# Kernel optimization log

Hardware: AMD Instinct MI355X
Metric: run time of the kernel (lower is better)

Reference implementation:

```python
import jax, jax.numpy as jnp
import numpy as np

N = 50000
E = 800000
D_IN, D_HID, D_OUT = 128, 128, 64


def setup_inputs() -> dict:
    key = jax.random.key(0)
    ks = jax.random.split(key, 8)
    x = jax.random.normal(ks[0], (N, D_IN), dtype=jnp.float32)
    edge_index = jax.random.randint(ks[1], (2, E), 0, N, dtype=jnp.int64)
    # SAGEConv params: lin_l (neighbors, with bias), lin_r (root, no bias)
    s1 = 1.0 / np.sqrt(D_IN)
    s2 = 1.0 / np.sqrt(D_HID)
    W1_l = jax.random.uniform(ks[2], (D_IN, D_HID), jnp.float32, -s1, s1)
    b1 = jnp.zeros((D_HID,), jnp.float32)
    W1_r = jax.random.uniform(ks[3], (D_IN, D_HID), jnp.float32, -s1, s1)
    W2_l = jax.random.uniform(ks[4], (D_HID, D_OUT), jnp.float32, -s2, s2)
    b2 = jnp.zeros((D_OUT,), jnp.float32)
    W2_r = jax.random.uniform(ks[5], (D_HID, D_OUT), jnp.float32, -s2, s2)
    return {"x": x, "edge_index": edge_index, "W1_l": W1_l, "b1": b1,
            "W1_r": W1_r, "W2_l": W2_l, "b2": b2, "W2_r": W2_r}


def _sage_conv(x, src, dst, Wl, b, Wr, num_nodes):
    # mean aggregation over incoming edges (src -> dst)
    msgs = x[src]                                              # [E, d]
    agg = jax.ops.segment_sum(msgs, dst, num_segments=num_nodes)
    cnt = jax.ops.segment_sum(jnp.ones((src.shape[0],), x.dtype), dst,
                              num_segments=num_nodes)
    mean = agg / jnp.clip(cnt, 1.0)[:, None]                   # [N, d]
    return mean @ Wl + b + x @ Wr


def reference(x, edge_index, W1_l, b1, W1_r, W2_l, b2, W2_r):
    src, dst = edge_index[0], edge_index[1]
    n = x.shape[0]
    h = jax.nn.relu(_sage_conv(x, src, dst, W1_l, b1, W1_r, n))
    # dropout p=0.5 is identity in eval mode (training=False)
    return _sage_conv(h, src, dst, W2_l, b2, W2_r, n)
```

## Files before the change

kernel.cpp:

```cpp
#include <hip/hip_runtime.h>
#include <hip/hip_bf16.h>

typedef __hip_bfloat16 bf16;
typedef __attribute__((ext_vector_type(8))) short short8;
typedef __attribute__((ext_vector_type(4))) float floatx4;
typedef __attribute__((ext_vector_type(2))) float floatx2;
typedef unsigned short u16;
typedef unsigned char u8;

#define NNODES 50000
#define NEDGES 800000
#define D_IN  128
#define D_HID 128
#define D_OUT 64
#define NBLK  ((NNODES + 255) / 256)

__device__ __forceinline__ float bfbits2f(unsigned int u) {
    return __uint_as_float(u << 16);
}
__device__ __forceinline__ float b2f(bf16 v) { return __bfloat162float(v); }
__device__ __forceinline__ unsigned short f2bfbits(float f) {
    bf16 b = __float2bfloat16(f);
    return *(unsigned short*)&b;
}
__device__ __forceinline__ u8 f2fp8(float f) {
    return (u8)(__builtin_amdgcn_cvt_pk_fp8_f32(f, 0.f, 0, false) & 0xFF);
}
__device__ __forceinline__ float ld(const void* p, long long idx, int isf32) {
    if (isf32) return ((const float*)p)[idx];
    return b2f(((const bf16*)p)[idx]);
}

__global__ void k_setup(int* __restrict__ cnt, int n,
                        const unsigned int* __restrict__ ei_words,
                        const unsigned int* __restrict__ w_words,
                        int* __restrict__ flags,
                        const void* __restrict__ x,
                        const void* __restrict__ W1l, const void* __restrict__ W1r,
                        const void* __restrict__ W2l, const void* __restrict__ W2r,
                        bf16* __restrict__ p1l, bf16* __restrict__ p1r,
                        bf16* __restrict__ p2l, bf16* __restrict__ p2r,
                        unsigned int* __restrict__ x8) {
    int b = blockIdx.x;
    if (b < 128) {
        if (b == 0) {
            __shared__ int cnt_zero, cnt_bf;
            if (threadIdx.x == 0) { cnt_zero = 0; cnt_bf = 0; }
            __syncthreads();
            int t = threadIdx.x;
            unsigned int we = ei_words[2 * t + 1];
            if (we == 0u) atomicAdd(&cnt_zero, 1);
            unsigned int ww = w_words[t];
            unsigned int lowexp = (ww >> 7) & 0xFFu;
            if (lowexp >= 0x60u && lowexp <= 0x7Bu) atomicAdd(&cnt_bf, 1);
            __syncthreads();
            if (threadIdx.x == 0) {
                flags[0] = (cnt_zero >= 240) ? 1 : 0;
                flags[1] = (cnt_bf >= 192) ? 0 : 1;
            }
        }
        int i = b * blockDim.x + threadIdx.x;
        int stride = 128 * blockDim.x;
        for (; i < n; i += stride) cnt[i] = 0;
        return;
    }
    __shared__ int cnt_bf2;
    if (threadIdx.x == 0) cnt_bf2 = 0;
    __syncthreads();
    {
        unsigned int ww = w_words[threadIdx.x];
        unsigned int lowexp = (ww >> 7) & 0xFFu;
        if (lowexp >= 0x60u && lowexp <= 0x7Bu) atomicAdd(&cnt_bf2, 1);
    }
    __syncthreads();
    int isf32 = (cnt_bf2 >= 192) ? 0 : 1;
    if (b < 152) {
        int t = (b - 128) * 256 + threadIdx.x;
        if (t >= 6144) return;
        const void* Wm; bf16* dst; int NT; int base;
        if (t < 2048)      { Wm = W1l; dst = p1l; NT = 8; base = t; }
        else if (t < 4096) { Wm = W1r; dst = p1r; NT = 8; base = t - 2048; }
        else if (t < 5120) { Wm = W2l; dst = p2l; NT = 4; base = t - 4096; }
        else               { Wm = W2r; dst = p2r; NT = 4; base = t - 5120; }
        int lane = base & 63;
        int kt = (base >> 6) & 3;
        int nt = base >> 8;
        int Nmat = NT * 16;
        int krow = kt * 32 + ((lane >> 4) * 8);
        int col = nt * 16 + (lane & 15);
        #pragma unroll
        for (int j = 0; j < 8; j++) {
            float v = ld(Wm, (long long)(krow + j) * Nmat + col, isf32);
            dst[(((nt * 4 + kt) * 64 + lane) * 8) + j] = __float2bfloat16(v);
        }
        return;
    }
    const long long NU32 = (long long)NNODES * D_IN / 4;
    long long i = (long long)(b - 152) * 256 + threadIdx.x;
    long long stride = (long long)(gridDim.x - 152) * 256;
    if (isf32) {
        const float4* xf = (const float4*)x;
        for (; i < NU32; i += stride) {
            float4 f = xf[i];
            unsigned int w0 = __builtin_amdgcn_cvt_pk_fp8_f32(f.x, f.y, 0, false);
            w0 = __builtin_amdgcn_cvt_pk_fp8_f32(f.z, f.w, w0, true);
            x8[i] = w0;
        }
    } else {
        const ushort4* xb = (const ushort4*)x;
        for (; i < NU32; i += stride) {
            ushort4 s = xb[i];
            float f0 = bfbits2f(s.x), f1 = bfbits2f(s.y);
            float f2 = bfbits2f(s.z), f3 = bfbits2f(s.w);
            unsigned int w0 = __builtin_amdgcn_cvt_pk_fp8_f32(f0, f1, 0, false);
            w0 = __builtin_amdgcn_cvt_pk_fp8_f32(f2, f3, w0, true);
            x8[i] = w0;
        }
    }
}

__global__ void k_edges(const int* __restrict__ ei, const int* __restrict__ flags,
                        u16* __restrict__ src16, unsigned int* __restrict__ drpack,
                        int* __restrict__ cnt) {
    int e = blockIdx.x * blockDim.x + threadIdx.x;
    if (e >= NEDGES) return;
    int s, d;
    if (flags[0]) { s = ei[2 * e]; d = ei[2 * (NEDGES + e)]; }
    else          { s = ei[e];     d = ei[NEDGES + e]; }
    src16[e] = (u16)s;
    int rank = atomicAdd(&cnt[d], 1);
    drpack[e] = ((unsigned int)rank << 16) | (unsigned int)d;
}

__global__ void k_scan_a(const int* __restrict__ cnt, int* __restrict__ excl,
                         int* __restrict__ bsum) {
    __shared__ int s[256];
    int t = threadIdx.x;
    int i = blockIdx.x * 256 + t;
    int v = (i < NNODES) ? cnt[i] : 0;
    s[t] = v;
    __syncthreads();
    for (int off = 1; off < 256; off <<= 1) {
        int u = (t >= off) ? s[t - off] : 0;
        __syncthreads();
        s[t] += u;
        __syncthreads();
    }
    if (i < NNODES) excl[i] = s[t] - v;
    if (t == 255) bsum[blockIdx.x] = s[255];
}

__global__ void k_scan_bc(const int* __restrict__ excl, const int* __restrict__ bsum,
                          int* __restrict__ row_start) {
    __shared__ int s[256];
    __shared__ int bo;
    int t = threadIdx.x;
    int v = (t < NBLK) ? bsum[t] : 0;
    s[t] = v;
    __syncthreads();
    for (int off = 1; off < 256; off <<= 1) {
        int u = (t >= off) ? s[t - off] : 0;
        __syncthreads();
        s[t] += u;
        __syncthreads();
    }
    if (t == 0) bo = s[blockIdx.x] - bsum[blockIdx.x];
    __syncthreads();
    int i = blockIdx.x * 256 + t;
    if (i < NNODES) row_start[i] = bo + excl[i];
    if (i == 0) row_start[NNODES] = NEDGES;
}

__global__ void k_scatter(const u16* __restrict__ src16,
                          const unsigned int* __restrict__ drpack,
                          const int* __restrict__ row_start,
                          u16* __restrict__ csr16) {
    int e = blockIdx.x * blockDim.x + threadIdx.x;
    if (e >= NEDGES) return;
    unsigned int dp = drpack[e];
    int d = (int)(dp & 0xFFFFu);
    int r = (int)(dp >> 16);
    csr16[row_start[d] + r] = src16[e];
}

__device__ __forceinline__ void g16m(const unsigned int* __restrict__ x8w, int my,
                                     int j, int cnt2, int h, int c,
                                     float& a0, float& a1, float& a2, float& a3) {
    int jb = j + h * 8;
    int i0 = __shfl(my, jb + 0), i1 = __shfl(my, jb + 1);
    int i2 = __shfl(my, jb + 2), i3 = __shfl(my, jb + 3);
    int i4 = __shfl(my, jb + 4), i5 = __shfl(my, jb + 5);
    int i6 = __shfl(my, jb + 6), i7 = __shfl(my, jb + 7);
    unsigned int u0 = x8w[((unsigned)i0 << 5) + c];
    unsigned int u1 = x8w[((unsigned)i1 << 5) + c];
    unsigned int u2 = x8w[((unsigned)i2 << 5) + c];
    unsigned int u3 = x8w[((unsigned)i3 << 5) + c];
    unsigned int u4 = x8w[((unsigned)i4 << 5) + c];
    unsigned int u5 = x8w[((unsigned)i5 << 5) + c];
    unsigned int u6 = x8w[((unsigned)i6 << 5) + c];
    unsigned int u7 = x8w[((unsigned)i7 << 5) + c];
    float m0 = (jb + 0 < cnt2) ? 1.f : 0.f;
    float m1 = (jb + 1 < cnt2) ? 1.f : 0.f;
    float m2 = (jb + 2 < cnt2) ? 1.f : 0.f;
    float m3 = (jb + 3 < cnt2) ? 1.f : 0.f;
    float m4 = (jb + 4 < cnt2) ? 1.f : 0.f;
    float m5 = (jb + 5 < cnt2) ? 1.f : 0.f;
    float m6 = (jb + 6 < cnt2) ? 1.f : 0.f;
    float m7 = (jb + 7 < cnt2) ? 1.f : 0.f;
    floatx2 l0 = __builtin_amdgcn_cvt_pk_f32_fp8(u0, false);
    floatx2 h0 = __builtin_amdgcn_cvt_pk_f32_fp8(u0, true);
    floatx2 l1 = __builtin_amdgcn_cvt_pk_f32_fp8(u1, false);
    floatx2 h1 = __builtin_amdgcn_cvt_pk_f32_fp8(u1, true);
    floatx2 l2 = __builtin_amdgcn_cvt_pk_f32_fp8(u2, false);
    floatx2 h2 = __builtin_amdgcn_cvt_pk_f32_fp8(u2, true);
    floatx2 l3 = __builtin_amdgcn_cvt_pk_f32_fp8(u3, false);
    floatx2 h3 = __builtin_amdgcn_cvt_pk_f32_fp8(u3, true);
    floatx2 l4 = __builtin_amdgcn_cvt_pk_f32_fp8(u4, false);
    floatx2 h4 = __builtin_amdgcn_cvt_pk_f32_fp8(u4, true);
    floatx2 l5 = __builtin_amdgcn_cvt_pk_f32_fp8(u5, false);
    floatx2 h5 = __builtin_amdgcn_cvt_pk_f32_fp8(u5, true);
    floatx2 l6 = __builtin_amdgcn_cvt_pk_f32_fp8(u6, false);
    floatx2 h6 = __builtin_amdgcn_cvt_pk_f32_fp8(u6, true);
    floatx2 l7 = __builtin_amdgcn_cvt_pk_f32_fp8(u7, false);
    floatx2 h7 = __builtin_amdgcn_cvt_pk_f32_fp8(u7, true);
    a0 += m0 * l0.x; a1 += m0 * l0.y; a2 += m0 * h0.x; a3 += m0 * h0.y;
    a0 += m1 * l1.x; a1 += m1 * l1.y; a2 += m1 * h1.x; a3 += m1 * h1.y;
    a0 += m2 * l2.x; a1 += m2 * l2.y; a2 += m2 * h2.x; a3 += m2 * h2.y;
    a0 += m3 * l3.x; a1 += m3 * l3.y; a2 += m3 * h3.x; a3 += m3 * h3.y;
    a0 += m4 * l4.x; a1 += m4 * l4.y; a2 += m4 * h4.x; a3 += m4 * h4.y;
    a0 += m5 * l5.x; a1 += m5 * l5.y; a2 += m5 * h5.x; a3 += m5 * h5.y;
    a0 += m6 * l6.x; a1 += m6 * l6.y; a2 += m6 * h6.x; a3 += m6 * h6.y;
    a0 += m7 * l7.x; a1 += m7 * l7.y; a2 += m7 * h7.x; a3 += m7 * h7.y;
}

__global__ __launch_bounds__(512) void k_l1fused(
        const int* __restrict__ row_start, const u16* __restrict__ csr16,
        const void* __restrict__ x, const unsigned int* __restrict__ x8w,
        const int* __restrict__ flags,
        const bf16* __restrict__ p1l, const bf16* __restrict__ p1r,
        const bf16* __restrict__ p2l, const bf16* __restrict__ p2r,
        const void* __restrict__ b1, const void* __restrict__ b2v,
        u8* __restrict__ h28, float* __restrict__ hrf) {
    __shared__ bf16 ms[16][136];
    __shared__ bf16 xs[16][136];
    __shared__ bf16 hs[16][136];
    __shared__ u8 h2s8[16][72];
    __shared__ float hrs[16][68];
    int t = threadIdx.x;
    int w = t >> 6;
    int l = t & 63;
    int nb = blockIdx.x * 16;
    int isf32 = flags[1];
    int r0 = w * 2, r1 = r0 + 1;
    int h = l >> 5;
    int c = l & 31;

    int rsv = row_start[nb + r0 + min(l, 2)];
    int s0 = __shfl(rsv, 0), s1 = __shfl(rsv, 1), s2 = __shfl(rsv, 2);

    int ca = min(64, s1 - s0);
    int cb = min(64, s2 - s1);
    int mya = (l < ca) ? (int)csr16[s0 + l] : 0;
    int myb = (l < cb) ? (int)csr16[s1 + l] : 0;

    {
        long long ro0 = (long long)(nb + r0) * D_IN + 2 * l;
        long long ro1 = (long long)(nb + r1) * D_IN + 2 * l;
        unsigned int px0, px1;
        if (isf32) {
            float2 v0 = *(const float2*)((const float*)x + ro0);
            float2 v1 = *(const float2*)((const float*)x + ro1);
            px0 = ((unsigned int)f2bfbits(v0.y) << 16) | f2bfbits(v0.x);
            px1 = ((unsigned int)f2bfbits(v1.y) << 16) | f2bfbits(v1.x);
        } else {
            px0 = *(const unsigned int*)((const bf16*)x + ro0);
            px1 = *(const unsigned int*)((const bf16*)x + ro1);
        }
        *(unsigned int*)((bf16*)&xs[r0][0] + 2 * l) = px0;
        *(unsigned int*)((bf16*)&xs[r1][0] + 2 * l) = px1;
    }

    float aa0 = 0.f, aa1 = 0.f, aa2 = 0.f, aa3 = 0.f;
    float bb0 = 0.f, bb1 = 0.f, bb2 = 0.f, bb3 = 0.f;
    {
        int mx = max(ca, cb);
        for (int j = 0; j < mx; j += 16) {
            g16m(x8w, mya, j, ca, h, c, aa0, aa1, aa2, aa3);
            g16m(x8w, myb, j, cb, h, c, bb0, bb1, bb2, bb3);
        }
    }
    for (int base = s0 + 64; base < s1; base += 64) {
        int cnt2 = min(64, s1 - base);
        int my = (l < cnt2) ? (int)csr16[base + l] : 0;
        for (int j = 0; j < cnt2; j += 16) g16m(x8w, my, j, cnt2, h, c, aa0, aa1, aa2, aa3);
    }
    for (int base = s1 + 64; base < s2; base += 64) {
        int cnt2 = min(64, s2 - base);
        int my = (l < cnt2) ? (int)csr16[base + l] : 0;
        for (int j = 0; j < cnt2; j += 16) g16m(x8w, my, j, cnt2, h, c, bb0, bb1, bb2, bb3);
    }
    aa0 += __shfl_xor(aa0, 32); aa1 += __shfl_xor(aa1, 32);
    aa2 += __shfl_xor(aa2, 32); aa3 += __shfl_xor(aa3, 32);
    bb0 += __shfl_xor(bb0, 32); bb1 += __shfl_xor(bb1, 32);
    bb2 += __shfl_xor(bb2, 32); bb3 += __shfl_xor(bb3, 32);
    if (l < 32) {
        float inv = 1.0f / fmaxf((float)(s1 - s0), 1.0f);
        uint2 pk;
        pk.x = ((unsigned int)f2bfbits(aa1 * inv) << 16) | f2bfbits(aa0 * inv);
        pk.y = ((unsigned int)f2bfbits(aa3 * inv) << 16) | f2bfbits(aa2 * inv);
        *(uint2*)((bf16*)&ms[r0][0] + (c << 2)) = pk;
    } else {
        float inv = 1.0f / fmaxf((float)(s2 - s1), 1.0f);
        uint2 pk;
        pk.x = ((unsigned int)f2bfbits(bb1 * inv) << 16) | f2bfbits(bb0 * inv);
        pk.y = ((unsigned int)f2bfbits(bb3 * inv) << 16) | f2bfbits(bb2 * inv);
        *(uint2*)((bf16*)&ms[r1][0] + (c << 2)) = pk;
    }
    __syncthreads();

    int m = l & 15;
    int quad = l >> 4;
    floatx4 acc0 = {0.f, 0.f, 0.f, 0.f};
    #pragma unroll
    for (int kt = 0; kt < 4; kt++) {
        short8 amv = *(const short8*)&ms[m][kt * 32 + quad * 8];
        short8 axv = *(const short8*)&xs[m][kt * 32 + quad * 8];
        short8 bl0 = *(const short8*)(p1l + (((w * 4 + kt) * 64 + l) * 8));
        short8 br0 = *(const short8*)(p1r + (((w * 4 + kt) * 64 + l) * 8));
        acc0 = __builtin_amdgcn_mfma_f32_16x16x32_bf16(amv, bl0, acc0, 0, 0, 0);
        acc0 = __builtin_amdgcn_mfma_f32_16x16x32_bf16(axv, br0, acc0, 0, 0, 0);
    }
    int c0 = w * 16 + m;
    float bias0 = ld(b1, c0, isf32);
    #pragma unroll
    for (int r = 0; r < 4; r++) {
        hs[quad * 4 + r][c0] = __float2bfloat16(fmaxf(acc0[r] + bias0, 0.f));
    }
    __syncthreads();
    if (w < 4) {
        floatx4 acc2 = {0.f, 0.f, 0.f, 0.f};
        floatx4 acc3 = {0.f, 0.f, 0.f, 0.f};
        #pragma unroll
        for (int kt = 0; kt < 4; kt++) {
            short8 ah = *(const short8*)&hs[m][kt * 32 + quad * 8];
            short8 bw = *(const short8*)(p2l + (((w * 4 + kt) * 64 + l) * 8));
            short8 bz = *(const short8*)(p2r + (((w * 4 + kt) * 64 + l) * 8));
            acc2 = __builtin_amdgcn_mfma_f32_16x16x32_bf16(ah, bw, acc2, 0, 0, 0);
            acc3 = __builtin_amdgcn_mfma_f32_16x16x32_bf16(ah, bz, acc3, 0, 0, 0);
        }
        int c2 = w * 16 + m;
        float bias2 = ld(b2v, c2, isf32);
        #pragma unroll
        for (int r = 0; r < 4; r++) {
            h2s8[quad * 4 + r][c2] = f2fp8(acc2[r]);
            hrs[quad * 4 + r][c2] = acc3[r] + bias2;
        }
    }
    __syncthreads();
    if (t < 128) {
        int node = t >> 3, col0 = (t & 7) * 8;
        uint2 v = *(const uint2*)&h2s8[node][col0];
        *(uint2*)(h28 + (long long)(nb + node) * D_OUT + col0) = v;
    }
    if (t < 256) {
        int node = t >> 4, col0 = (t & 15) * 4;
        float4 v = *(const float4*)&hrs[node][col0];
        *(float4*)(hrf + (long long)(nb + node) * D_OUT + col0) = v;
    }
}

__device__ __forceinline__ void a16m(const unsigned int* __restrict__ h32, int my,
                                     int j, int cnt2, int g, int c,
                                     float& a0, float& a1, float& a2, float& a3) {
    int jj0 = j + g, jj1 = j + 4 + g, jj2 = j + 8 + g, jj3 = j + 12 + g;
    int i0 = __shfl(my, jj0);
    int i1 = __shfl(my, jj1);
    int i2 = __shfl(my, jj2);
    int i3 = __shfl(my, jj3);
    unsigned int u0 = h32[(size_t)i0 * 16 + c];
    unsigned int u1 = h32[(size_t)i1 * 16 + c];
    unsigned int u2 = h32[(size_t)i2 * 16 + c];
    unsigned int u3 = h32[(size_t)i3 * 16 + c];
    float m0 = (jj0 < cnt2) ? 1.f : 0.f;
    float m1 = (jj1 < cnt2) ? 1.f : 0.f;
    float m2 = (jj2 < cnt2) ? 1.f : 0.f;
    float m3 = (jj3 < cnt2) ? 1.f : 0.f;
    floatx2 l0 = __builtin_amdgcn_cvt_pk_f32_fp8(u0, false);
    floatx2 h0 = __builtin_amdgcn_cvt_pk_f32_fp8(u0, true);
    floatx2 l1 = __builtin_amdgcn_cvt_pk_f32_fp8(u1, false);
    floatx2 h1 = __builtin_amdgcn_cvt_pk_f32_fp8(u1, true);
    floatx2 l2 = __builtin_amdgcn_cvt_pk_f32_fp8(u2, false);
    floatx2 h2 = __builtin_amdgcn_cvt_pk_f32_fp8(u2, true);
    floatx2 l3 = __builtin_amdgcn_cvt_pk_f32_fp8(u3, false);
    floatx2 h3 = __builtin_amdgcn_cvt_pk_f32_fp8(u3, true);
    a0 += m0 * l0.x; a1 += m0 * l0.y; a2 += m0 * h0.x; a3 += m0 * h0.y;
    a0 += m1 * l1.x; a1 += m1 * l1.y; a2 += m1 * h1.x; a3 += m1 * h1.y;
    a0 += m2 * l2.x; a1 += m2 * l2.y; a2 += m2 * h2.x; a3 += m2 * h2.y;
    a0 += m3 * l3.x; a1 += m3 * l3.y; a2 += m3 * h3.x; a3 += m3 * h3.y;
}

__global__ void k_agg2g(const int* __restrict__ row_start, const u16* __restrict__ csr16,
                        const u8* __restrict__ h28, const float* __restrict__ hrf,
                        const int* __restrict__ flags, void* __restrict__ out) {
    int t = threadIdx.x;
    int lane = t & 63;
    int n0 = blockIdx.x * 8 + (t >> 6) * 2;
    int n1 = n0 + 1;
    int g = lane >> 4;
    int c = lane & 15;
    const unsigned int* h32 = (const unsigned int*)h28;

    int rsv = row_start[n0 + min(lane, 2)];
    int s0 = __shfl(rsv, 0), s1 = __shfl(rsv, 1), s2 = __shfl(rsv, 2);
    int ca = min(64, s1 - s0);
    int cb = min(64, s2 - s1);
    int mya = (lane < ca) ? (int)csr16[s0 + lane] : 0;
    int myb = (lane < cb) ? (int)csr16[s1 + lane] : 0;

    float4 hr = {0.f, 0.f, 0.f, 0.f};
    if (lane < 32) {
        int nn = (lane < 16) ? n0 : n1;
        hr = *(const float4*)&hrf[(size_t)nn * D_OUT + (c << 2)];
    }

    float a0 = 0.f, a1 = 0.f, a2 = 0.f, a3 = 0.f;
    float b0 = 0.f, b1 = 0.f, b2 = 0.f, b3 = 0.f;
    {
        int mx = max(ca, cb);
        for (int j = 0; j < mx; j += 16) {
            a16m(h32, mya, j, ca, g, c, a0, a1, a2, a3);
            a16m(h32, myb, j, cb, g, c, b0, b1, b2, b3);
        }
    }
    for (int base = s0 + 64; base < s1; base += 64) {
        int cnt2 = min(64, s1 - base);
        int my = (lane < cnt2) ? (int)csr16[base + lane] : 0;
        for (int j = 0; j < cnt2; j += 16) a16m(h32, my, j, cnt2, g, c, a0, a1, a2, a3);
    }
    for (int base = s1 + 64; base < s2; base += 64) {
        int cnt2 = min(64, s2 - base);
        int my = (lane < cnt2) ? (int)csr16[base + lane] : 0;
        for (int j = 0; j < cnt2; j += 16) a16m(h32, my, j, cnt2, g, c, b0, b1, b2, b3);
    }
    a0 += __shfl_xor(a0, 32); a0 += __shfl_xor(a0, 16);
    a1 += __shfl_xor(a1, 32); a1 += __shfl_xor(a1, 16);
    a2 += __shfl_xor(a2, 32); a2 += __shfl_xor(a2, 16);
    a3 += __shfl_xor(a3, 32); a3 += __shfl_xor(a3, 16);
    b0 += __shfl_xor(b0, 32); b0 += __shfl_xor(b0, 16);
    b1 += __shfl_xor(b1, 32); b1 += __shfl_xor(b1, 16);
    b2 += __shfl_xor(b2, 32); b2 += __shfl_xor(b2, 16);
    b3 += __shfl_xor(b3, 32); b3 += __shfl_xor(b3, 16);
    if (lane < 16) {
        float inv = 1.0f / fmaxf((float)(s1 - s0), 1.0f);
        float o0 = a0 * inv + hr.x;
        float o1 = a1 * inv + hr.y;
        float o2 = a2 * inv + hr.z;
        float o3 = a3 * inv + hr.w;
        if (flags[1]) {
            float4 v = {o0, o1, o2, o3};
            *(float4*)((float*)out + (size_t)n0 * D_OUT + (c << 2)) = v;
        } else {
            uint2 v;
            v.x = ((unsigned int)f2bfbits(o1) << 16) | f2bfbits(o0);
            v.y = ((unsigned int)f2bfbits(o3) << 16) | f2bfbits(o2);
            *(uint2*)((bf16*)out + (size_t)n0 * D_OUT + (c << 2)) = v;
        }
    } else if (lane < 32) {
        float inv = 1.0f / fmaxf((float)(s2 - s1), 1.0f);
        float o0 = b0 * inv + hr.x;
        float o1 = b1 * inv + hr.y;
        float o2 = b2 * inv + hr.z;
        float o3 = b3 * inv + hr.w;
        if (flags[1]) {
            float4 v = {o0, o1, o2, o3};
            *(float4*)((float*)out + (size_t)n1 * D_OUT + (c << 2)) = v;
        } else {
            uint2 v;
            v.x = ((unsigned int)f2bfbits(o1) << 16) | f2bfbits(o0);
            v.y = ((unsigned int)f2bfbits(o3) << 16) | f2bfbits(o2);
            *(uint2*)((bf16*)out + (size_t)n1 * D_OUT + (c << 2)) = v;
        }
    }
}

extern "C" void kernel_launch(void* const* d_in, const int* in_sizes, int n_in,
                              void* d_out, int out_size, void* d_ws, size_t ws_size,
                              hipStream_t stream) {
    const void* x   = d_in[0];
    const int*  ei  = (const int*)d_in[1];
    const void* W1l = d_in[2];
    const void* b1  = d_in[3];
    const void* W1r = d_in[4];
    const void* W2l = d_in[5];
    const void* b2v = d_in[6];
    const void* W2r = d_in[7];

    const int N = NNODES;
    const int E = NEDGES;

    int*          flags     = (int*)d_ws;
    u16*          src16     = (u16*)(flags + 4);
    unsigned int* drpack    = (unsigned int*)(src16 + E);
    int*          cnt       = (int*)(drpack + E);
    int*          excl      = cnt + N;
    int*          bsum      = excl + N;
    int*          row_start = bsum + 256;
    u16*          csr16     = (u16*)(row_start + (N + 16));
    bf16*         p1l       = (bf16*)(csr16 + E);
    bf16*         p1r       = p1l + 16384;
    bf16*         p2l       = p1r + 16384;
    bf16*         p2r       = p2l + 8192;
    unsigned int* x8        = (unsigned int*)(p2r + 8192);
    u8*           h28       = (u8*)(x8 + (size_t)N * D_IN / 4);
    float*        hrf       = (float*)(h28 + (size_t)N * D_OUT);

    k_setup<<<152 + 1024, 256, 0, stream>>>(cnt, N, (const unsigned int*)ei,
                                            (const unsigned int*)W1l, flags, x,
                                            W1l, W1r, W2l, W2r,
                                            p1l, p1r, p2l, p2r, x8);
    k_edges<<<(E + 255) / 256, 256, 0, stream>>>(ei, flags, src16, drpack, cnt);
    k_scan_a<<<NBLK, 256, 0, stream>>>(cnt, excl, bsum);
    k_scan_bc<<<NBLK, 256, 0, stream>>>(excl, bsum, row_start);
    k_scatter<<<(E + 255) / 256, 256, 0, stream>>>(src16, drpack, row_start, csr16);
    k_l1fused<<<N / 16, 512, 0, stream>>>(row_start, csr16, x, x8, flags,
                                          p1l, p1r, p2l, p2r, b1, b2v, h28, hrf);
    k_agg2g<<<N / 8, 256, 0, stream>>>(row_start, csr16, h28, hrf, flags, d_out);
}
```

Measured before the change: 196.2 us.

## Process two node tiles per layer-1 block and four nodes per warp in aggregation

The fused layer-1 kernel now handles two 16-node tiles per block, prefetching the second tile's row starts, neighbor indices and root features while the first tile's MFMA work runs, which halves the block count and reuses weight loads. The layer-2 aggregation kernel gives each warp four destination nodes instead of two, issuing more independent gathers per loop iteration for memory-level parallelism. The cost is higher register pressure and longer serial work per block, which may reduce occupancy and worsen load imbalance on high-degree nodes.

```diff
diff --git a/kernel.cpp b/kernel.cpp
--- a/kernel.cpp
+++ b/kernel.cpp
@@ -249,23 +249,25 @@
     int t = threadIdx.x;
     int w = t >> 6;
     int l = t & 63;
-    int nb = blockIdx.x * 16;
     int isf32 = flags[1];
     int r0 = w * 2, r1 = r0 + 1;
     int h = l >> 5;
     int c = l & 31;
-
-    int rsv = row_start[nb + r0 + min(l, 2)];
+    int m = l & 15;
+    int quad = l >> 4;
+    int nbA = blockIdx.x * 32;
+    int nbB = nbA + 16;
+    bool hasB = (nbB < NNODES);
+
+    int rsv = row_start[nbA + r0 + min(l, 2)];
     int s0 = __shfl(rsv, 0), s1 = __shfl(rsv, 1), s2 = __shfl(rsv, 2);
-
     int ca = min(64, s1 - s0);
     int cb = min(64, s2 - s1);
     int mya = (l < ca) ? (int)csr16[s0 + l] : 0;
     int myb = (l < cb) ? (int)csr16[s1 + l] : 0;
-
     {
-        long long ro0 = (long long)(nb + r0) * D_IN + 2 * l;
-        long long ro1 = (long long)(nb + r1) * D_IN + 2 * l;
+        long long ro0 = (long long)(nbA + r0) * D_IN + 2 * l;
+        long long ro1 = (long long)(nbA + r1) * D_IN + 2 * l;
         unsigned int px0, px1;
         if (isf32) {
             float2 v0 = *(const float2*)((const float*)x + ro0);
@@ -299,6 +301,10 @@
         int my = (l < cnt2) ? (int)csr16[base + l] : 0;
         for (int j = 0; j < cnt2; j += 16) g16m(x8w, my, j, cnt2, h, c, bb0, bb1, bb2, bb3);
     }
+
+    int rsvB = 0;
+    if (hasB) rsvB = row_start[nbB + r0 + min(l, 2)];
+
     aa0 += __shfl_xor(aa0, 32); aa1 += __shfl_xor(aa1, 32);
     aa2 += __shfl_xor(aa2, 32); aa3 += __shfl_xor(aa3, 32);
     bb0 += __shfl_xor(bb0, 32); bb1 += __shfl_xor(bb1, 32);
@@ -318,23 +324,45 @@
     }
     __syncthreads();
 
-    int m = l & 15;
-    int quad = l >> 4;
-    floatx4 acc0 = {0.f, 0.f, 0.f, 0.f};
-    #pragma unroll
-    for (int kt = 0; kt < 4; kt++) {
-        short8 amv = *(const short8*)&ms[m][kt * 32 + quad * 8];
-        short8 axv = *(const short8*)&xs[m][kt * 32 + quad * 8];
-        short8 bl0 = *(const short8*)(p1l + (((w * 4 + kt) * 64 + l) * 8));
-        short8 br0 = *(const short8*)(p1r + (((w * 4 + kt) * 64 + l) * 8));
-        acc0 = __builtin_amdgcn_mfma_f32_16x16x32_bf16(amv, bl0, acc0, 0, 0, 0);
-        acc0 = __builtin_amdgcn_mfma_f32_16x16x32_bf16(axv, br0, acc0, 0, 0, 0);
-    }
-    int c0 = w * 16 + m;
-    float bias0 = ld(b1, c0, isf32);
-    #pragma unroll
-    for (int r = 0; r < 4; r++) {
-        hs[quad * 4 + r][c0] = __float2bfloat16(fmaxf(acc0[r] + bias0, 0.f));
+    int s0B = 0, s1B = 0, s2B = 0, caB = 0, cbB = 0;
+    int myaB = 0, mybB = 0;
+    unsigned int pxB0 = 0, pxB1 = 0;
+    if (hasB) {
+        s0B = __shfl(rsvB, 0); s1B = __shfl(rsvB, 1); s2B = __shfl(rsvB, 2);
+        caB = min(64, s1B - s0B);
+        cbB = min(64, s2B - s1B);
+        myaB = (l < caB) ? (int)csr16[s0B + l] : 0;
+        mybB = (l < cbB) ? (int)csr16[s1B + l] : 0;
+        long long ro0 = (long long)(nbB + r0) * D_IN + 2 * l;
+        long long ro1 = (long long)(nbB + r1) * D_IN + 2 * l;
+        if (isf32) {
+            float2 v0 = *(const float2*)((const float*)x + ro0);
+            float2 v1 = *(const float2*)((const float*)x + ro1);
+            pxB0 = ((unsigned int)f2bfbits(v0.y) << 16) | f2bfbits(v0.x);
+            pxB1 = ((unsigned int)f2bfbits(v1.y) << 16) | f2bfbits(v1.x);
+        } else {
+            pxB0 = *(const unsigned int*)((const bf16*)x + ro0);
+            pxB1 = *(const unsigned int*)((const bf16*)x + ro1);
+        }
+    }
+
+    {
+        floatx4 acc0 = {0.f, 0.f, 0.f, 0.f};
+        #pragma unroll
+        for (int kt = 0; kt < 4; kt++) {
+            short8 amv = *(const short8*)&ms[m][kt * 32 + quad * 8];
+            short8 axv = *(const short8*)&xs[m][kt * 32 + quad * 8];
+            short8 bl0 = *(const short8*)(p1l + (((w * 4 + kt) * 64 + l) * 8));
+            short8 br0 = *(const short8*)(p1r + (((w * 4 + kt) * 64 + l) * 8));
+            acc0 = __builtin_amdgcn_mfma_f32_16x16x32_bf16(amv, bl0, acc0, 0, 0, 0);
+            acc0 = __builtin_amdgcn_mfma_f32_16x16x32_bf16(axv, br0, acc0, 0, 0, 0);
+        }
+        int c0 = w * 16 + m;
+        float bias0 = ld(b1, c0, isf32);
+        #pragma unroll
+        for (int r = 0; r < 4; r++) {
+            hs[quad * 4 + r][c0] = __float2bfloat16(fmaxf(acc0[r] + bias0, 0.f));
+        }
     }
     __syncthreads();
     if (w < 4) {
@@ -360,12 +388,104 @@
     if (t < 128) {
         int node = t >> 3, col0 = (t & 7) * 8;
         uint2 v = *(const uint2*)&h2s8[node][col0];
-        *(uint2*)(h28 + (long long)(nb + node) * D_OUT + col0) = v;
+        *(uint2*)(h28 + (long long)(nbA + node) * D_OUT + col0) = v;
     }
     if (t < 256) {
         int node = t >> 4, col0 = (t & 15) * 4;
         float4 v = *(const float4*)&hrs[node][col0];
-        *(float4*)(hrf + (long long)(nb + node) * D_OUT + col0) = v;
+        *(float4*)(hrf + (long long)(nbA + node) * D_OUT + col0) = v;
+    }
+
+    if (!hasB) return;
+
+    *(unsigned int*)((bf16*)&xs[r0][0] + 2 * l) = pxB0;
+    *(unsigned int*)((bf16*)&xs[r1][0] + 2 * l) = pxB1;
+
+    float ca0 = 0.f, ca1 = 0.f, ca2 = 0.f, ca3 = 0.f;
+    float cb0 = 0.f, cb1 = 0.f, cb2 = 0.f, cb3 = 0.f;
+    {
+        int mx = max(caB, cbB);
+        for (int j = 0; j < mx; j += 16) {
+            g16m(x8w, myaB, j, caB, h, c, ca0, ca1, ca2, ca3);
+            g16m(x8w, mybB, j, cbB, h, c, cb0, cb1, cb2, cb3);
+        }
+    }
+    for (int base = s0B + 64; base < s1B; base += 64) {
+        int cnt2 = min(64, s1B - base);
+        int my = (l < cnt2) ? (int)csr16[base + l] : 0;
+        for (int j = 0; j < cnt2; j += 16) g16m(x8w, my, j, cnt2, h, c, ca0, ca1, ca2, ca3);
+    }
+    for (int base = s1B + 64; base < s2B; base += 64) {
+        int cnt2 = min(64, s2B - base);
+        int my = (l < cnt2) ? (int)csr16[base + l] : 0;
+        for (int j = 0; j < cnt2; j += 16) g16m(x8w, my, j, cnt2, h, c, cb0, cb1, cb2, cb3);
+    }
+    ca0 += __shfl_xor(ca0, 32); ca1 += __shfl_xor(ca1, 32);
+    ca2 += __shfl_xor(ca2, 32); ca3 += __shfl_xor(ca3, 32);
+    cb0 += __shfl_xor(cb0, 32); cb1 += __shfl_xor(cb1, 32);
+    cb2 += __shfl_xor(cb2, 32); cb3 += __shfl_xor(cb3, 32);
+    if (l < 32) {
+        float inv = 1.0f / fmaxf((float)(s1B - s0B), 1.0f);
+        uint2 pk;
+        pk.x = ((unsigned int)f2bfbits(ca1 * inv) << 16) | f2bfbits(ca0 * inv);
+        pk.y = ((unsigned int)f2bfbits(ca3 * inv) << 16) | f2bfbits(ca2 * inv);
+        *(uint2*)((bf16*)&ms[r0][0] + (c << 2)) = pk;
+    } else {
+        float inv = 1.0f / fmaxf((float)(s2B - s1B), 1.0f);
+        uint2 pk;
+        pk.x = ((unsigned int)f2bfbits(cb1 * inv) << 16) | f2bfbits(cb0 * inv);
+        pk.y = ((unsigned int)f2bfbits(cb3 * inv) << 16) | f2bfbits(cb2 * inv);
+        *(uint2*)((bf16*)&ms[r1][0] + (c << 2)) = pk;
+    }
+    __syncthreads();
+    {
+        floatx4 acc0 = {0.f, 0.f, 0.f, 0.f};
+        #pragma unroll
+        for (int kt = 0; kt < 4; kt++) {
+            short8 amv = *(const short8*)&ms[m][kt * 32 + quad * 8];
+            short8 axv = *(const short8*)&xs[m][kt * 32 + quad * 8];
+            short8 bl0 = *(const short8*)(p1l + (((w * 4 + kt) * 64 + l) * 8));
+            short8 br0 = *(const short8*)(p1r + (((w * 4 + kt) * 64 + l) * 8));
+            acc0 = __builtin_amdgcn_mfma_f32_16x16x32_bf16(amv, bl0, acc0, 0, 0, 0);
+            acc0 = __builtin_amdgcn_mfma_f32_16x16x32_bf16(axv, br0, acc0, 0, 0, 0);
+        }
+        int c0 = w * 16 + m;
+        float bias0 = ld(b1, c0, isf32);
+        #pragma unroll
+        for (int r = 0; r < 4; r++) {
+            hs[quad * 4 + r][c0] = __float2bfloat16(fmaxf(acc0[r] + bias0, 0.f));
+        }
+    }
+    __syncthreads();
+    if (w < 4) {
+        floatx4 acc2 = {0.f, 0.f, 0.f, 0.f};
+        floatx4 acc3 = {0.f, 0.f, 0.f, 0.f};
+        #pragma unroll
+        for (int kt = 0; kt < 4; kt++) {
+            short8 ah = *(const short8*)&hs[m][kt * 32 + quad * 8];
+            short8 bw = *(const short8*)(p2l + (((w * 4 + kt) * 64 + l) * 8));
+            short8 bz = *(const short8*)(p2r + (((w * 4 + kt) * 64 + l) * 8));
+            acc2 = __builtin_amdgcn_mfma_f32_16x16x32_bf16(ah, bw, acc2, 0, 0, 0);
+            acc3 = __builtin_amdgcn_mfma_f32_16x16x32_bf16(ah, bz, acc3, 0, 0, 0);
+        }
+        int c2 = w * 16 + m;
+        float bias2 = ld(b2v, c2, isf32);
+        #pragma unroll
+        for (int r = 0; r < 4; r++) {
+            h2s8[quad * 4 + r][c2] = f2fp8(acc2[r]);
+            hrs[quad * 4 + r][c2] = acc3[r] + bias2;
+        }
+    }
+    __syncthreads();
+    if (t < 128) {
+        int node = t >> 3, col0 = (t & 7) * 8;
+        uint2 v = *(const uint2*)&h2s8[node][col0];
+        *(uint2*)(h28 + (long long)(nbB + node) * D_OUT + col0) = v;
+    }
+    if (t < 256) {
+        int node = t >> 4, col0 = (t & 15) * 4;
+        float4 v = *(const float4*)&hrs[node][col0];
+        *(float4*)(hrf + (long long)(nbB + node) * D_OUT + col0) = v;
     }
 }
 
@@ -404,82 +524,91 @@
                         const int* __restrict__ flags, void* __restrict__ out) {
     int t = threadIdx.x;
     int lane = t & 63;
-    int n0 = blockIdx.x * 8 + (t >> 6) * 2;
-    int n1 = n0 + 1;
+    int base = blockIdx.x * 16 + (t >> 6) * 4;
     int g = lane >> 4;
     int c = lane & 15;
     const unsigned int* h32 = (const unsigned int*)h28;
 
-    int rsv = row_start[n0 + min(lane, 2)];
+    int rsv = row_start[base + min(lane, 4)];
     int s0 = __shfl(rsv, 0), s1 = __shfl(rsv, 1), s2 = __shfl(rsv, 2);
-    int ca = min(64, s1 - s0);
-    int cb = min(64, s2 - s1);
-    int mya = (lane < ca) ? (int)csr16[s0 + lane] : 0;
-    int myb = (lane < cb) ? (int)csr16[s1 + lane] : 0;
-
-    float4 hr = {0.f, 0.f, 0.f, 0.f};
-    if (lane < 32) {
-        int nn = (lane < 16) ? n0 : n1;
-        hr = *(const float4*)&hrf[(size_t)nn * D_OUT + (c << 2)];
-    }
-
-    float a0 = 0.f, a1 = 0.f, a2 = 0.f, a3 = 0.f;
-    float b0 = 0.f, b1 = 0.f, b2 = 0.f, b3 = 0.f;
-    {
-        int mx = max(ca, cb);
-        for (int j = 0; j < mx; j += 16) {
-            a16m(h32, mya, j, ca, g, c, a0, a1, a2, a3);
-            a16m(h32, myb, j, cb, g, c, b0, b1, b2, b3);
-        }
-    }
-    for (int base = s0 + 64; base < s1; base += 64) {
-        int cnt2 = min(64, s1 - base);
-        int my = (lane < cnt2) ? (int)csr16[base + lane] : 0;
-        for (int j = 0; j < cnt2; j += 16) a16m(h32, my, j, cnt2, g, c, a0, a1, a2, a3);
-    }
-    for (int base = s1 + 64; base < s2; base += 64) {
-        int cnt2 = min(64, s2 - base);
-        int my = (lane < cnt2) ? (int)csr16[base + lane] : 0;
-        for (int j = 0; j < cnt2; j += 16) a16m(h32, my, j, cnt2, g, c, b0, b1, b2, b3);
-    }
-    a0 += __shfl_xor(a0, 32); a0 += __shfl_xor(a0, 16);
-    a1 += __shfl_xor(a1, 32); a1 += __shfl_xor(a1, 16);
-    a2 += __shfl_xor(a2, 32); a2 += __shfl_xor(a2, 16);
-    a3 += __shfl_xor(a3, 32); a3 += __shfl_xor(a3, 16);
-    b0 += __shfl_xor(b0, 32); b0 += __shfl_xor(b0, 16);
-    b1 += __shfl_xor(b1, 32); b1 += __shfl_xor(b1, 16);
-    b2 += __shfl_xor(b2, 32); b2 += __shfl_xor(b2, 16);
-    b3 += __shfl_xor(b3, 32); b3 += __shfl_xor(b3, 16);
-    if (lane < 16) {
-        float inv = 1.0f / fmaxf((float)(s1 - s0), 1.0f);
-        float o0 = a0 * inv + hr.x;
-        float o1 = a1 * inv + hr.y;
-        float o2 = a2 * inv + hr.z;
-        float o3 = a3 * inv + hr.w;
-        if (flags[1]) {
-            float4 v = {o0, o1, o2, o3};
-            *(float4*)((float*)out + (size_t)n0 * D_OUT + (c << 2)) = v;
-        } else {
-            uint2 v;
-            v.x = ((unsigned int)f2bfbits(o1) << 16) | f2bfbits(o0);
-            v.y = ((unsigned int)f2bfbits(o3) << 16) | f2bfbits(o2);
-            *(uint2*)((bf16*)out + (size_t)n0 * D_OUT + (c << 2)) = v;
-        }
-    } else if (lane < 32) {
-        float inv = 1.0f / fmaxf((float)(s2 - s1), 1.0f);
-        float o0 = b0 * inv + hr.x;
-        float o1 = b1 * inv + hr.y;
-        float o2 = b2 * inv + hr.z;
-        float o3 = b3 * inv + hr.w;
-        if (flags[1]) {
-            float4 v = {o0, o1, o2, o3};
-            *(float4*)((float*)out + (size_t)n1 * D_OUT + (c << 2)) = v;
-        } else {
-            uint2 v;
-            v.x = ((unsigned int)f2bfbits(o1) << 16) | f2bfbits(o0);
-            v.y = ((unsigned int)f2bfbits(o3) << 16) | f2bfbits(o2);
-            *(uint2*)((bf16*)out + (size_t)n1 * D_OUT + (c << 2)) = v;
-        }
+    int s3 = __shfl(rsv, 3), s4 = __shfl(rsv, 4);
+    int c0n = min(64, s1 - s0);
+    int c1n = min(64, s2 - s1);
+    int c2n = min(64, s3 - s2);
+    int c3n = min(64, s4 - s3);
+    int my0 = (lane < c0n) ? (int)csr16[s0 + lane] : 0;
+    int my1 = (lane < c1n) ? (int)csr16[s1 + lane] : 0;
+    int my2 = (lane < c2n) ? (int)csr16[s2 + lane] : 0;
+    int my3 = (lane < c3n) ? (int)csr16[s3 + lane] : 0;
+    float4 hr = *(const float4*)&hrf[(size_t)(base + g) * D_OUT + (c << 2)];
+
+    float A0 = 0.f, A1 = 0.f, A2 = 0.f, A3 = 0.f;
+    float B0 = 0.f, B1 = 0.f, B2 = 0.f, B3 = 0.f;
+    float C0 = 0.f, C1 = 0.f, C2 = 0.f, C3 = 0.f;
+    float D0 = 0.f, D1 = 0.f, D2 = 0.f, D3 = 0.f;
+    int mx = max(max(c0n, c1n), max(c2n, c3n));
+    for (int j = 0; j < mx; j += 16) {
+        a16m(h32, my0, j, c0n, g, c, A0, A1, A2, A3);
+        a16m(h32, my1, j, c1n, g, c, B0, B1, B2, B3);
+        a16m(h32, my2, j, c2n, g, c, C0, C1, C2, C3);
+        a16m(h32, my3, j, c3n, g, c, D0, D1, D2, D3);
+    }
+    for (int b2 = s0 + 64; b2 < s1; b2 += 64) {
+        int cnt2 = min(64, s1 - b2);
+        int my = (lane < cnt2) ? (int)csr16[b2 + lane] : 0;
+        for (int j = 0; j < cnt2; j += 16) a16m(h32, my, j, cnt2, g, c, A0, A1, A2, A3);
+    }
+    for (int b2 = s1 + 64; b2 < s2; b2 += 64) {
+        int cnt2 = min(64, s2 - b2);
+        int my = (lane < cnt2) ? (int)csr16[b2 + lane] : 0;
+        for (int j = 0; j < cnt2; j += 16) a16m(h32, my, j, cnt2, g, c, B0, B1, B2, B3);
+    }
+    for (int b2 = s2 + 64; b2 < s3; b2 += 64) {
+        int cnt2 = min(64, s3 - b2);
+        int my = (lane < cnt2) ? (int)csr16[b2 + lane] : 0;
+        for (int j = 0; j < cnt2; j += 16) a16m(h32, my, j, cnt2, g, c, C0, C1, C2, C3);
+    }
+    for (int b2 = s3 + 64; b2 < s4; b2 += 64) {
+        int cnt2 = min(64, s4 - b2);
+        int my = (lane < cnt2) ? (int)csr16[b2 + lane] : 0;
+        for (int j = 0; j < cnt2; j += 16) a16m(h32, my, j, cnt2, g, c, D0, D1, D2, D3);
+    }
+    A0 += __shfl_xor(A0, 32); A0 += __shfl_xor(A0, 16);
+    A1 += __shfl_xor(A1, 32); A1 += __shfl_xor(A1, 16);
+    A2 += __shfl_xor(A2, 32); A2 += __shfl_xor(A2, 16);
+    A3 += __shfl_xor(A3, 32); A3 += __shfl_xor(A3, 16);
+    B0 += __shfl_xor(B0, 32); B0 += __shfl_xor(B0, 16);
+    B1 += __shfl_xor(B1, 32); B1 += __shfl_xor(B1, 16);
+    B2 += __shfl_xor(B2, 32); B2 += __shfl_xor(B2, 16);
+    B3 += __shfl_xor(B3, 32); B3 += __shfl_xor(B3, 16);
+    C0 += __shfl_xor(C0, 32); C0 += __shfl_xor(C0, 16);
+    C1 += __shfl_xor(C1, 32); C1 += __shfl_xor(C1, 16);
+    C2 += __shfl_xor(C2, 32); C2 += __shfl_xor(C2, 16);
+    C3 += __shfl_xor(C3, 32); C3 += __shfl_xor(C3, 16);
+    D0 += __shfl_xor(D0, 32); D0 += __shfl_xor(D0, 16);
+    D1 += __shfl_xor(D1, 32); D1 += __shfl_xor(D1, 16);
+    D2 += __shfl_xor(D2, 32); D2 += __shfl_xor(D2, 16);
+    D3 += __shfl_xor(D3, 32); D3 += __shfl_xor(D3, 16);
+    float o0 = (g == 0) ? A0 : (g == 1) ? B0 : (g == 2) ? C0 : D0;
+    float o1 = (g == 0) ? A1 : (g == 1) ? B1 : (g == 2) ? C1 : D1;
+    float o2 = (g == 0) ? A2 : (g == 1) ? B2 : (g == 2) ? C2 : D2;
+    float o3 = (g == 0) ? A3 : (g == 1) ? B3 : (g == 2) ? C3 : D3;
+    float dg = (g == 0) ? (float)(s1 - s0) : (g == 1) ? (float)(s2 - s1)
+             : (g == 2) ? (float)(s3 - s2) : (float)(s4 - s3);
+    float inv = 1.0f / fmaxf(dg, 1.0f);
+    o0 = o0 * inv + hr.x;
+    o1 = o1 * inv + hr.y;
+    o2 = o2 * inv + hr.z;
+    o3 = o3 * inv + hr.w;
+    size_t off = (size_t)(base + g) * D_OUT + (c << 2);
+    if (flags[1]) {
+        float4 v = {o0, o1, o2, o3};
+        *(float4*)((float*)out + off) = v;
+    } else {
+        uint2 v;
+        v.x = ((unsigned int)f2bfbits(o1) << 16) | f2bfbits(o0);
+        v.y = ((unsigned int)f2bfbits(o3) << 16) | f2bfbits(o2);
+        *(uint2*)((bf16*)out + off) = v;
     }
 }
 
@@ -522,7 +651,7 @@
     k_scan_a<<<NBLK, 256, 0, stream>>>(cnt, excl, bsum);
     k_scan_bc<<<NBLK, 256, 0, stream>>>(excl, bsum, row_start);
     k_scatter<<<(E + 255) / 256, 256, 0, stream>>>(src16, drpack, row_start, csr16);
-    k_l1fused<<<N / 16, 512, 0, stream>>>(row_start, csr16, x, x8, flags,
-                                          p1l, p1r, p2l, p2r, b1, b2v, h28, hrf);
-    k_agg2g<<<N / 8, 256, 0, stream>>>(row_start, csr16, h28, hrf, flags, d_out);
-}
+    k_l1fused<<<(N + 31) / 32, 512, 0, stream>>>(row_start, csr16, x, x8, flags,
+                                                 p1l, p1r, p2l, p2r, b1, b2v, h28, hrf);
+    k_agg2g<<<N / 16, 256, 0, stream>>>(row_start, csr16, h28, hrf, flags, d_out);
+}
```

Measured after the change: 204.4 us. 4.1% more time.
